# Performance work log

Hardware: AMD Instinct MI355X
Metric: run time of the kernel (lower is better)

Reference implementation:

```python
import jax, jax.numpy as jnp
import numpy as np
from jax import lax

POOL_K, POOL_S, FINAL, KNN = 5, 3, 6, 819  # pool size/stride, adaptive out, k_neighbors


def setup_inputs() -> dict:
    key = jax.random.key(0)
    k1, k2, k3 = jax.random.split(key, 3)
    return {
        "x": jax.random.normal(k1, (64, 3, 32, 32), jnp.float32),
        "conv_weight": jax.random.normal(k2, (2048, 3, 6, 6), jnp.float32) * 0.05,
        "conv_bias": jax.random.normal(k3, (1, 2048, 1, 1), jnp.float32),
    }


def lowestk_heaviside(x, k):
    # indicator of the k channel-wise smallest values: x < (k+1)-th smallest
    kth = jnp.sort(x, axis=1)[:, k:k + 1]  # [B,1,H,W]
    return (x < kth).astype(x.dtype)


def avg_pool_ceil(x, k, s):
    # torch avg_pool2d(ceil_mode=True, padding=0): partial windows clipped to
    # the input and divided by the number of valid elements.
    H, W = x.shape[2], x.shape[3]
    oh = -(-(H - k) // s) + 1
    ow = -(-(W - k) // s) + 1
    ph = max(0, (oh - 1) * s + k - H)
    pw = max(0, (ow - 1) * s + k - W)
    dims, strides = (1, 1, k, k), (1, 1, s, s)
    pad = ((0, 0), (0, 0), (0, ph), (0, pw))
    sums = lax.reduce_window(x, 0.0, lax.add, dims, strides, pad)
    cnt = lax.reduce_window(jnp.ones((1, 1, H, W), x.dtype), 0.0, lax.add,
                            dims, strides, pad)
    return sums / cnt


def adaptive_avg_pool2d(x, n):
    # torch adaptive bins: [floor(i*S/n), ceil((i+1)*S/n)); separable in H/W
    def pool_axis(y, axis):
        size = y.shape[axis]
        parts = []
        for i in range(n):
            s = (i * size) // n
            e = -(-((i + 1) * size) // n)
            parts.append(lax.slice_in_dim(y, s, e, axis=axis)
                         .mean(axis=axis, keepdims=True))
        return jnp.concatenate(parts, axis=axis)
    return pool_axis(pool_axis(x, 2), 3)


def reference(x, conv_weight, conv_bias):
    out = lax.conv_general_dilated(x, conv_weight, (1, 1), 'VALID',
                                   dimension_numbers=('NCHW', 'OIHW', 'NCHW'))

    def branch(z):
        m = lowestk_heaviside(z, KNN)            # [B,2048,27,27]
        m = avg_pool_ceil(m, POOL_K, POOL_S)     # [B,2048,9,9]
        return adaptive_avg_pool2d(m, FINAL)     # [B,2048,6,6]

    out1 = branch(-out + conv_bias)
    out2 = branch(out + conv_bias)
    return (out1, out2)
```

## Files before the change

kernel.cpp:

```cpp
#include <hip/hip_runtime.h>
#include <cstdint>
#include <cstddef>

#define RANK_K 819

typedef __attribute__((ext_vector_type(2))) float f32x2;

__device__ __forceinline__ f32x2 pk_fma_blo(f32x2 a, f32x2 bs, f32x2 c) {
  f32x2 d;
  asm("v_pk_fma_f32 %0, %1, %2, %3 op_sel_hi:[1,0,1]"
      : "=v"(d) : "v"(a), "s"(bs), "v"(c));
  return d;
}
__device__ __forceinline__ f32x2 pk_fma_bhi(f32x2 a, f32x2 bs, f32x2 c) {
  f32x2 d;
  asm("v_pk_fma_f32 %0, %1, %2, %3 op_sel:[0,1,0] op_sel_hi:[1,1,1]"
      : "=v"(d) : "v"(a), "s"(bs), "v"(c));
  return d;
}

#define RFL(v) __int_as_float(__builtin_amdgcn_readfirstlane(__float_as_int(v)))

__device__ __forceinline__ int zbin256(float z) {
  float t = (z + 8.0f) * 16.0f;
  t = t < 0.0f ? 0.0f : (t > 255.0f ? 255.0f : t);
  return (int)t;
}

__global__ __launch_bounds__(256) void net99_wtrans(const float* __restrict__ w,
                                                    f32x2* __restrict__ wt4) {
  int idx = blockIdx.x * 256 + threadIdx.x;
  if (idx < 108 * 1024) {
    int k = idx / 1024, cc = idx % 1024;
    int ic = k % 3, sp = k / 3, ky = sp / 6, kx = sp % 6;
    int wo = ic * 36 + ky * 6 + kx;
    f32x2 t;
    t.x = w[cc * 108 + wo];
    t.y = w[(cc + 1024) * 108 + wo];
    wt4[idx] = t;
  }
}

__global__ __launch_bounds__(256) void net99_conv(const float* __restrict__ x,
                                                  const f32x2* __restrict__ wt4,
                                                  float* __restrict__ conv, int b0) {
  const int y  = blockIdx.x;
  const int ct = blockIdx.y;
  const int bl = blockIdx.z;
  const int b  = b0 + bl;
  const int tid = threadIdx.x;
  __shared__ __align__(16) float xs[3][6][32];
  for (int i = tid; i < 576; i += 256) {
    int ic = i / 192, rem = i % 192, r = rem / 32, col = rem % 32;
    xs[ic][r][col] = x[((b * 3 + ic) * 32 + (y + r)) * 32 + col];
  }
  __syncthreads();
  const int cpair = ct * 256 + tid;
  const f32x2* wtc = wt4 + cpair;
  f32x2 acc[27];
#pragma unroll
  for (int q = 0; q < 27; ++q) acc[q] = (f32x2)(0.0f);
#pragma unroll 1
  for (int ky = 0; ky < 6; ++ky) {
    f32x2 xpair[3][16];
#pragma unroll
    for (int ic = 0; ic < 3; ++ic) {
      const float4* rp = (const float4*)(&xs[ic][ky][0]);
#pragma unroll
      for (int j = 0; j < 8; ++j) {
        float4 f = rp[j];
        f32x2 plo, phi;
        plo.x = RFL(f.x); plo.y = RFL(f.y);
        phi.x = RFL(f.z); phi.y = RFL(f.w);
        xpair[ic][2 * j]     = plo;
        xpair[ic][2 * j + 1] = phi;
      }
    }
#pragma unroll
    for (int kx = 0; kx < 6; ++kx) {
#pragma unroll
      for (int ic = 0; ic < 3; ++ic) {
        f32x2 wv = wtc[(size_t)((ky * 6 + kx) * 3 + ic) * 1024];
#pragma unroll
        for (int q = 0; q < 27; ++q) {
          const int col = kx + q;
          f32x2 xp = xpair[ic][col >> 1];
          acc[q] = (col & 1) ? pk_fma_bhi(wv, xp, acc[q])
                             : pk_fma_blo(wv, xp, acc[q]);
        }
      }
    }
  }
  float* dstbase = conv + ((size_t)(bl * 27 + y) * 27) * 2048;
#pragma unroll
  for (int q = 0; q < 27; ++q) {
    dstbase[(size_t)q * 2048 + cpair]        = acc[q].x;
    dstbase[(size_t)q * 2048 + cpair + 1024] = acc[q].y;
  }
}

__global__ __launch_bounds__(256, 2) void net99_select(const float* __restrict__ conv,
                                                       const float* __restrict__ bias,
                                                       uint8_t* __restrict__ mskb, int b0) {
  const int bl = blockIdx.x / 183;
  const int g  = blockIdx.x % 183;
  const int p0 = 4 * g;
  const int npix = (g < 182) ? 4 : 1;
  const int nst  = 2 * npix;
  const int gb = b0 + bl;
  const int tid  = threadIdx.x;
  const int lane = tid & 63;
  const int wid  = tid >> 6;
  __shared__ uint32_t hist[8][256];
  __shared__ float    cand[8][512];
  __shared__ int      cnt[8];
  __shared__ int      sbin[8], sbelow[8];
  __shared__ float    skth[8];

  const float4* __restrict__ s0 =
      (const float4*)(conv + ((size_t)bl * 729 + p0) * 2048) + tid * 2;
  const float4* __restrict__ b4 = (const float4*)bias + tid * 2;
  float4 va[4][2];
#pragma unroll
  for (int k = 0; k < 4; ++k) {
    if (k < npix) { va[k][0] = s0[k * 512]; va[k][1] = s0[k * 512 + 1]; }
    else          { va[k][0] = float4{0,0,0,0}; va[k][1] = float4{0,0,0,0}; }
  }
  float4 ba = b4[0], bb = b4[1];

#pragma unroll
  for (int r = 0; r < 8; ++r) (&hist[0][0])[tid + 256 * r] = 0u;
  if (tid < 8) cnt[tid] = 0;

  float z[8][8];
  {
    float bv[8] = {ba.x, ba.y, ba.z, ba.w, bb.x, bb.y, bb.z, bb.w};
#pragma unroll
    for (int k = 0; k < 4; ++k) {
      float v[8] = {va[k][0].x, va[k][0].y, va[k][0].z, va[k][0].w,
                    va[k][1].x, va[k][1].y, va[k][1].z, va[k][1].w};
#pragma unroll
      for (int j = 0; j < 8; ++j) {
        z[2 * k][j]     = bv[j] - v[j];
        z[2 * k + 1][j] = bv[j] + v[j];
      }
    }
  }
  __syncthreads();
#pragma unroll
  for (int s = 0; s < 8; ++s) {
    if (s < nst) {
#pragma unroll
      for (int j = 0; j < 8; ++j) atomicAdd(&hist[s][zbin256(z[s][j])], 1u);
    }
  }
  __syncthreads();
#pragma unroll
  for (int rep = 0; rep < 2; ++rep) {
    const int s = wid + 4 * rep;
    if (s < nst) {
      int h[4];
#pragma unroll
      for (int t = 0; t < 4; ++t) h[t] = (int)hist[s][lane * 4 + t];
      int loc = h[0] + h[1] + h[2] + h[3];
      int inc = loc;
#pragma unroll
      for (int off = 1; off < 64; off <<= 1) {
        int u = __shfl_up(inc, off);
        if (lane >= off) inc += u;
      }
      int pre = inc - loc;
      if (pre <= RANK_K && RANK_K < pre + loc) {
        int cum = pre;
#pragma unroll
        for (int t = 0; t < 4; ++t) {
          if (RANK_K < cum + h[t]) { sbin[s] = lane * 4 + t; sbelow[s] = cum; break; }
          cum += h[t];
        }
      }
    }
  }
  __syncthreads();
#pragma unroll
  for (int s = 0; s < 8; ++s) {
    if (s < nst) {
      const int tb = sbin[s];
#pragma unroll
      for (int j = 0; j < 8; ++j) {
        if (zbin256(z[s][j]) == tb) {
          int u = atomicAdd(&cnt[s], 1);
          if (u < 512) cand[s][u] = z[s][j];
        }
      }
    }
  }
  __syncthreads();
#pragma unroll
  for (int rep = 0; rep < 2; ++rep) {
    const int s = wid + 4 * rep;
    if (s < nst) {
      int cN = cnt[s] < 512 ? cnt[s] : 512;
      int rloc = RANK_K - sbelow[s];
      for (int ci = lane; ci < cN; ci += 64) {
        float v = cand[s][ci]; int rk = 0;
        for (int j = 0; j < cN; ++j) {
          float u = cand[s][j];
          rk += (u < v) || (u == v && j < ci);
        }
        if (rk == rloc) skth[s] = v;
      }
    }
  }
  __syncthreads();
#pragma unroll
  for (int k = 0; k < 4; ++k) {
    if (k < npix) {
      uint32_t m0 = 0u, m1 = 0u;
      const float k0 = skth[2 * k], k1 = skth[2 * k + 1];
#pragma unroll
      for (int j = 0; j < 8; ++j) {
        m0 |= (uint32_t)(z[2 * k][j] < k0) << j;
        m1 |= (uint32_t)(z[2 * k + 1][j] < k1) << j;
      }
      const size_t pix = (size_t)gb * 729 + p0 + k;
      mskb[pix * 256 + tid]                      = (uint8_t)m0;
      mskb[((size_t)64 * 729 + pix) * 256 + tid] = (uint8_t)m1;
    }
  }
}

__global__ __launch_bounds__(256) void net99_pool(const uint32_t* __restrict__ msk,
                                                  float* __restrict__ out) {
  __shared__ uint32_t stage[729 * 8];
  const int blk = blockIdx.x;
  const int cg  = blk & 7;
  const int sb  = blk >> 3;
  const int tid = threadIdx.x;
  const uint32_t* src = msk + (size_t)sb * 729 * 64 + cg * 8;
  for (int i = tid; i < 729 * 8; i += 256) {
    int p = i >> 3, w = i & 7;
    stage[i] = src[(size_t)p * 64 + w];
  }
  __syncthreads();
  const int lw = tid >> 5, sel = tid & 31;
  uint32_t rbm[27];
  for (int y = 0; y < 27; ++y) {
    uint32_t rb = 0;
#pragma unroll
    for (int xx = 0; xx < 27; ++xx)
      rb |= ((stage[(y * 27 + xx) * 8 + lw] >> sel) & 1u) << xx;
    rbm[y] = rb;
  }
  constexpr uint32_t WM[9] = {0x1Fu, 0xF8u, 0x7C0u, 0x3E00u, 0x1F000u,
                              0xF8000u, 0x7C0000u, 0x3E00000u, 0x7000000u};
  constexpr int CC[9]  = {5, 5, 5, 5, 5, 5, 5, 5, 3};
  constexpr int BW0[6] = {0, 1, 3, 4, 6, 7};
  constexpr int BW1[6] = {1, 2, 4, 5, 7, 8};
  const int s = sb >> 6, b = sb & 63, c = cg * 256 + tid;
  float* dst = out + (size_t)s * 4718592 + (size_t)(b * 2048 + c) * 36;
  for (int i = 0; i < 6; ++i) {
    float P[2][9];
#pragma unroll
    for (int t = 0; t < 2; ++t) {
      int r  = t ? BW1[i] : BW0[i];
      int y0 = 3 * r;
      int y1 = (y0 + 5 > 27) ? 27 : y0 + 5;
      int cr = y1 - y0;
      int pp[9];
#pragma unroll
      for (int cx = 0; cx < 9; ++cx) pp[cx] = 0;
      for (int yy = y0; yy < y1; ++yy) {
        uint32_t rb = rbm[yy];
#pragma unroll
        for (int cx = 0; cx < 9; ++cx) pp[cx] += __popc(rb & WM[cx]);
      }
#pragma unroll
      for (int cx = 0; cx < 9; ++cx)
        P[t][cx] = (float)pp[cx] / (float)(cr * CC[cx]);
    }
    float M[9];
#pragma unroll
    for (int cx = 0; cx < 9; ++cx) M[cx] = (P[0][cx] + P[1][cx]) * 0.5f;
#pragma unroll
    for (int j = 0; j < 6; ++j)
      dst[i * 6 + j] = (M[BW0[j]] + M[BW1[j]]) * 0.5f;
  }
}

extern "C" void kernel_launch(void* const* d_in, const int* in_sizes, int n_in,
                              void* d_out, int out_size, void* d_ws, size_t ws_size,
                              hipStream_t stream) {
  const float* x    = (const float*)d_in[0];
  const float* w    = (const float*)d_in[1];
  const float* bias = (const float*)d_in[2];
  float* out = (float*)d_out;
  uint8_t* ws = (uint8_t*)d_ws;

  const size_t WT_BYTES   = (size_t)108 * 1024 * 8;
  const size_t MASK_OFF   = WT_BYTES;
  const size_t MASK_BYTES = (size_t)2 * 64 * 729 * 64 * 4;
  const size_t CONV_OFF   = MASK_OFF + MASK_BYTES;
  const size_t PER_B      = (size_t)2048 * 729 * 4;

  f32x2*    wt4  = (f32x2*)ws;
  uint8_t*  mskb = (uint8_t*)(ws + MASK_OFF);
  uint32_t* msk  = (uint32_t*)(ws + MASK_OFF);
  float*    conv = (float*)(ws + CONV_OFF);

  size_t avail = ws_size > CONV_OFF ? ws_size - CONV_OFF : 0;
  int Bc = (int)(avail / PER_B);
  if (Bc < 1) Bc = 1;
  if (Bc > 64) Bc = 64;

  hipLaunchKernelGGL(net99_wtrans, dim3((108 * 1024 + 255) / 256), dim3(256), 0, stream, w, wt4);
  for (int b0 = 0; b0 < 64; b0 += Bc) {
    int nb = (64 - b0 < Bc) ? (64 - b0) : Bc;
    hipLaunchKernelGGL(net99_conv, dim3(27, 4, nb), dim3(256), 0, stream, x, wt4, conv, b0);
    hipLaunchKernelGGL(net99_select, dim3(nb * 183), dim3(256), 0, stream, conv, bias, mskb, b0);
  }
  hipLaunchKernelGGL(net99_pool, dim3(1024), dim3(256), 0, stream, msk, out);
}
```

Baseline: 482.7 us.

## Load conv input rows via scalar loads instead of LDS staging with readfirstlane

The conv kernel stops staging input rows in shared memory, dropping the __syncthreads and the per-element readfirstlane moves. Each ky iteration now reads input rows directly into SGPRs with s_load_dwordx16. It preloads all 18 weight pairs per ky and reorders the FMA loop to iterate over input columns, with occupancy hinted at 4 blocks per CU. The cost is an explicit lgkmcnt(0) wait after each scalar load and higher register pressure from the preloaded weights, which could conflict with the raised occupancy target.

Result: no change. 475.6 us (-1.5%).

```diff
diff --git a/kernel.cpp b/kernel.cpp
--- a/kernel.cpp
+++ b/kernel.cpp
@@ -4,7 +4,15 @@
 
 #define RANK_K 819
 
-typedef __attribute__((ext_vector_type(2))) float f32x2;
+typedef __attribute__((ext_vector_type(2)))  float f32x2;
+typedef __attribute__((ext_vector_type(16))) float f32x16;
+
+__device__ __forceinline__ f32x16 sload16(const float* p) {
+  f32x16 r;
+  asm volatile("s_load_dwordx16 %0, %1, 0x0\n\ts_waitcnt lgkmcnt(0)"
+               : "=s"(r) : "s"(p));
+  return r;
+}
 
 __device__ __forceinline__ f32x2 pk_fma_blo(f32x2 a, f32x2 bs, f32x2 c) {
   f32x2 d;
@@ -18,8 +26,6 @@
       : "=v"(d) : "v"(a), "s"(bs), "v"(c));
   return d;
 }
-
-#define RFL(v) __int_as_float(__builtin_amdgcn_readfirstlane(__float_as_int(v)))
 
 __device__ __forceinline__ int zbin256(float z) {
   float t = (z + 8.0f) * 16.0f;
@@ -41,20 +47,14 @@
   }
 }
 
-__global__ __launch_bounds__(256) void net99_conv(const float* __restrict__ x,
-                                                  const f32x2* __restrict__ wt4,
-                                                  float* __restrict__ conv, int b0) {
+__global__ __launch_bounds__(256, 4) void net99_conv(const float* __restrict__ x,
+                                                     const f32x2* __restrict__ wt4,
+                                                     float* __restrict__ conv, int b0) {
   const int y  = blockIdx.x;
   const int ct = blockIdx.y;
   const int bl = blockIdx.z;
   const int b  = b0 + bl;
   const int tid = threadIdx.x;
-  __shared__ __align__(16) float xs[3][6][32];
-  for (int i = tid; i < 576; i += 256) {
-    int ic = i / 192, rem = i % 192, r = rem / 32, col = rem % 32;
-    xs[ic][r][col] = x[((b * 3 + ic) * 32 + (y + r)) * 32 + col];
-  }
-  __syncthreads();
   const int cpair = ct * 256 + tid;
   const f32x2* wtc = wt4 + cpair;
   f32x2 acc[27];
@@ -62,31 +62,63 @@
   for (int q = 0; q < 27; ++q) acc[q] = (f32x2)(0.0f);
 #pragma unroll 1
   for (int ky = 0; ky < 6; ++ky) {
-    f32x2 xpair[3][16];
-#pragma unroll
-    for (int ic = 0; ic < 3; ++ic) {
-      const float4* rp = (const float4*)(&xs[ic][ky][0]);
-#pragma unroll
-      for (int j = 0; j < 8; ++j) {
-        float4 f = rp[j];
-        f32x2 plo, phi;
-        plo.x = RFL(f.x); plo.y = RFL(f.y);
-        phi.x = RFL(f.z); phi.y = RFL(f.w);
-        xpair[ic][2 * j]     = plo;
-        xpair[ic][2 * j + 1] = phi;
-      }
-    }
-#pragma unroll
-    for (int kx = 0; kx < 6; ++kx) {
-#pragma unroll
-      for (int ic = 0; ic < 3; ++ic) {
-        f32x2 wv = wtc[(size_t)((ky * 6 + kx) * 3 + ic) * 1024];
-#pragma unroll
-        for (int q = 0; q < 27; ++q) {
-          const int col = kx + q;
-          f32x2 xp = xpair[ic][col >> 1];
-          acc[q] = (col & 1) ? pk_fma_bhi(wv, xp, acc[q])
-                             : pk_fma_blo(wv, xp, acc[q]);
+    const float* r0 = x + ((b * 3 + 0) * 32 + (y + ky)) * 32;
+    const float* r1 = x + ((b * 3 + 1) * 32 + (y + ky)) * 32;
+    const float* r2 = x + ((b * 3 + 2) * 32 + (y + ky)) * 32;
+    f32x2 wv[6][3];
+#pragma unroll
+    for (int kx = 0; kx < 6; ++kx)
+#pragma unroll
+      for (int ic = 0; ic < 3; ++ic)
+        wv[kx][ic] = wtc[(size_t)((ky * 6 + kx) * 3 + ic) * 1024];
+    {
+      f32x16 a0 = sload16(r0), a1 = sload16(r1), a2 = sload16(r2);
+#pragma unroll
+      for (int m = 0; m < 16; ++m) {
+        f32x2 p0, p1, p2;
+        p0.x = a0[(m >> 1) * 2]; p0.y = a0[(m >> 1) * 2 + 1];
+        p1.x = a1[(m >> 1) * 2]; p1.y = a1[(m >> 1) * 2 + 1];
+        p2.x = a2[(m >> 1) * 2]; p2.y = a2[(m >> 1) * 2 + 1];
+#pragma unroll
+        for (int kx = 0; kx < 6; ++kx) {
+          if (kx <= m) {
+            const int q = m - kx;
+            if (m & 1) {
+              acc[q] = pk_fma_bhi(wv[kx][0], p0, acc[q]);
+              acc[q] = pk_fma_bhi(wv[kx][1], p1, acc[q]);
+              acc[q] = pk_fma_bhi(wv[kx][2], p2, acc[q]);
+            } else {
+              acc[q] = pk_fma_blo(wv[kx][0], p0, acc[q]);
+              acc[q] = pk_fma_blo(wv[kx][1], p1, acc[q]);
+              acc[q] = pk_fma_blo(wv[kx][2], p2, acc[q]);
+            }
+          }
+        }
+      }
+    }
+    {
+      f32x16 c0 = sload16(r0 + 16), c1 = sload16(r1 + 16), c2 = sload16(r2 + 16);
+#pragma unroll
+      for (int m = 16; m < 32; ++m) {
+        const int mm = m - 16;
+        f32x2 p0, p1, p2;
+        p0.x = c0[(mm >> 1) * 2]; p0.y = c0[(mm >> 1) * 2 + 1];
+        p1.x = c1[(mm >> 1) * 2]; p1.y = c1[(mm >> 1) * 2 + 1];
+        p2.x = c2[(mm >> 1) * 2]; p2.y = c2[(mm >> 1) * 2 + 1];
+#pragma unroll
+        for (int kx = 0; kx < 6; ++kx) {
+          const int q = m - kx;
+          if (q <= 26) {
+            if (m & 1) {
+              acc[q] = pk_fma_bhi(wv[kx][0], p0, acc[q]);
+              acc[q] = pk_fma_bhi(wv[kx][1], p1, acc[q]);
+              acc[q] = pk_fma_bhi(wv[kx][2], p2, acc[q]);
+            } else {
+              acc[q] = pk_fma_blo(wv[kx][0], p0, acc[q]);
+              acc[q] = pk_fma_blo(wv[kx][1], p1, acc[q]);
+              acc[q] = pk_fma_blo(wv[kx][2], p2, acc[q]);
+            }
+          }
         }
       }
     }
```
